# Optimization experiments

Hardware: AMD Instinct MI355X
Metric: run time of the kernel (lower is better)

Reference implementation:

```python
import jax, jax.numpy as jnp
import numpy as np

DIM = 512
N_LABELS = 64


def setup_inputs() -> dict:
    key = jax.random.key(0)
    k1, k2, k3, k4 = jax.random.split(key, 4)
    head = jax.random.normal(k1, (8, 512, DIM), dtype=jnp.float32)
    dep = jax.random.normal(k2, (8, 512, DIM), dtype=jnp.float32)
    label_W = jax.random.normal(k3, (N_LABELS, 2 * DIM), dtype=jnp.float32) * 0.02
    label_b = jax.random.normal(k4, (N_LABELS,), dtype=jnp.float32) * 0.02
    return {"head": head, "dep": dep, "label_W": label_W, "label_b": label_b}


def reference(head, dep, label_W, label_b):
    # Original: concated[b, i*S+j] = concat(head[b,i], dep[b,j]) -> [B, S*S, 2D]
    #           out = (label_W @ concated^T).view(B, L, S, S) + b
    # Fused biaffine decomposition: out[b,l,i,j] = Wh[l].head[b,i] + Wd[l].dep[b,j] + b[l]
    D = head.shape[-1]
    W_head = label_W[:, :D]   # [L, D]
    W_dep = label_W[:, D:]    # [L, D]
    h = jnp.einsum('bid,ld->bli', head, W_head)  # [B, L, S]
    d = jnp.einsum('bjd,ld->blj', dep, W_dep)    # [B, L, S]
    out = h[:, :, :, None] + d[:, :, None, :] + label_b[None, :, None, None]
    return out  # [B, L, S, S]
```

## Files before the change

kernel.cpp:

```cpp
#include <hip/hip_runtime.h>
#include <hip/hip_bf16.h>

#define BATCH 8
#define SEQ   512
#define DIM   512
#define NL    64
#define ITILE 16

typedef float f32x4 __attribute__((ext_vector_type(4)));

__global__ __launch_bounds__(256) void alab_proj(
    const float* __restrict__ head, const float* __restrict__ dep,
    const float* __restrict__ W, const float* __restrict__ bias,
    float* __restrict__ hbuf, float* __restrict__ dbuf)
{
    __shared__ float4 sh[ITILE * (DIM / 4)];
    __shared__ float4 sd[ITILE * (DIM / 4)];
    const int t  = threadIdx.x;
    const int b  = blockIdx.x >> 5;
    const int i0 = (blockIdx.x & 31) * ITILE;

    const float4* h4 = (const float4*)(head + ((size_t)b * SEQ + i0) * DIM);
    const float4* d4 = (const float4*)(dep  + ((size_t)b * SEQ + i0) * DIM);
    #pragma unroll
    for (int u = t; u < ITILE * (DIM / 4); u += 256) {
        const int row = u >> 7, col = u & 127;
        const int sc  = col ^ (row & 7);
        sh[row * 128 + sc] = h4[u];
        sd[row * 128 + sc] = d4[u];
    }
    __syncthreads();

    const int iL = t & 15;
    const int lg = t >> 4;
    const int xm = iL & 7;
    const float4* W4 = (const float4*)W;

    float acch[4] = {0.f, 0.f, 0.f, 0.f};
    float accd[4] = {0.f, 0.f, 0.f, 0.f};
    for (int k4 = 0; k4 < DIM / 4; ++k4) {
        const float4 hv = sh[iL * 128 + (k4 ^ xm)];
        const float4 dv = sd[iL * 128 + (k4 ^ xm)];
        #pragma unroll
        for (int r = 0; r < 4; ++r) {
            const int l = lg * 4 + r;
            const float4 wh = W4[l * 256 + k4];
            const float4 wd = W4[l * 256 + 128 + k4];
            acch[r] += wh.x * hv.x + wh.y * hv.y + wh.z * hv.z + wh.w * hv.w;
            accd[r] += wd.x * dv.x + wd.y * dv.y + wd.z * dv.z + wd.w * dv.w;
        }
    }

    #pragma unroll
    for (int r = 0; r < 4; ++r) {
        const int l = lg * 4 + r;
        const size_t o = ((size_t)b * NL + l) * SEQ + i0 + iL;
        hbuf[o] = acch[r] + bias[l];
        dbuf[o] = accd[r];
    }
}

__global__ __launch_bounds__(256) void alab_bcast3(
    const float* __restrict__ hbuf, const float* __restrict__ dbuf,
    float* __restrict__ out)
{
    __shared__ float sh[SEQ / 4];
    __shared__ f32x4 sd4[SEQ / 4];
    const int t  = threadIdx.x;
    const int q  = blockIdx.x & 3;
    const int bl = blockIdx.x >> 2;

    if (t < 128) sh[t] = hbuf[(size_t)bl * SEQ + q * 128 + t];
    ((float*)sd4)[t]       = dbuf[(size_t)bl * SEQ + t];
    ((float*)sd4)[t + 256] = dbuf[(size_t)bl * SEQ + t + 256];
    __syncthreads();

    const int j4 = t & 127;
    const int rh = t >> 7;
    const f32x4 dreg = sd4[j4];
    f32x4* ob = (f32x4*)out + ((size_t)bl * SEQ + q * 128) * (SEQ / 4);

    #pragma unroll 8
    for (int ii = 0; ii < 128; ii += 2) {
        const int i = ii + rh;
        const f32x4 o = dreg + sh[i];
        ob[(size_t)i * (SEQ / 4) + j4] = o;
    }
}

extern "C" void kernel_launch(void* const* d_in, const int* in_sizes, int n_in,
                              void* d_out, int out_size, void* d_ws, size_t ws_size,
                              hipStream_t stream) {
    const float* head = (const float*)d_in[0];
    const float* dep  = (const float*)d_in[1];
    const float* W    = (const float*)d_in[2];
    const float* bias = (const float*)d_in[3];
    float* out  = (float*)d_out;
    float* hbuf = (float*)d_ws;
    float* dbuf = hbuf + (size_t)BATCH * NL * SEQ;

    alab_proj<<<BATCH * (SEQ / ITILE), 256, 0, stream>>>(head, dep, W, bias, hbuf, dbuf);
    alab_bcast3<<<BATCH * NL * 4, 256, 0, stream>>>(hbuf, dbuf, out);
}
```

Measured before the change: 135.9 us.

## Split projection kernel into separate head/dep blocks with padded LDS and vector accumulators

The projection kernel now launches twice as many blocks, each handling only the head or only the dep half. Each block stages one 16-row tile in padded shared memory instead of an XOR swizzle and accumulates with f32x4 vector FMAs, reducing lanes only at the end. The aim is more parallelism and lower per-block shared memory for the small projection stage. The cost is fewer W loads amortized per block, and the per-block LDS reads change pattern.

```diff
diff --git a/kernel.cpp b/kernel.cpp
--- a/kernel.cpp
+++ b/kernel.cpp
@@ -5,58 +5,60 @@
 #define SEQ   512
 #define DIM   512
 #define NL    64
-#define ITILE 16
 
 typedef float f32x4 __attribute__((ext_vector_type(4)));
 
-__global__ __launch_bounds__(256) void alab_proj(
+__global__ __launch_bounds__(256) void alab_proj2(
     const float* __restrict__ head, const float* __restrict__ dep,
     const float* __restrict__ W, const float* __restrict__ bias,
     float* __restrict__ hbuf, float* __restrict__ dbuf)
 {
-    __shared__ float4 sh[ITILE * (DIM / 4)];
-    __shared__ float4 sd[ITILE * (DIM / 4)];
-    const int t  = threadIdx.x;
-    const int b  = blockIdx.x >> 5;
-    const int i0 = (blockIdx.x & 31) * ITILE;
+    __shared__ float4 srow[16][129];
+    const int bid   = blockIdx.x;
+    const int hd    = bid & 1;
+    const int itile = (bid >> 1) & 31;
+    const int b     = bid >> 6;
+    const int i0    = itile * 16;
 
-    const float4* h4 = (const float4*)(head + ((size_t)b * SEQ + i0) * DIM);
-    const float4* d4 = (const float4*)(dep  + ((size_t)b * SEQ + i0) * DIM);
+    const float* src  = hd ? dep  : head;
+    float*       dst  = hd ? dbuf : hbuf;
+    const int    wofs = hd ? 128  : 0;
+
+    const float4* s4 = (const float4*)(src + ((size_t)b * SEQ + i0) * DIM);
     #pragma unroll
-    for (int u = t; u < ITILE * (DIM / 4); u += 256) {
-        const int row = u >> 7, col = u & 127;
-        const int sc  = col ^ (row & 7);
-        sh[row * 128 + sc] = h4[u];
-        sd[row * 128 + sc] = d4[u];
-    }
+    for (int u = threadIdx.x; u < 16 * 128; u += 256)
+        srow[u >> 7][u & 127] = s4[u];
     __syncthreads();
 
-    const int iL = t & 15;
-    const int lg = t >> 4;
-    const int xm = iL & 7;
-    const float4* W4 = (const float4*)W;
+    const int lane = threadIdx.x & 63;
+    const int w    = threadIdx.x >> 6;
+    const int i    = lane & 15;
+    const int li   = lane >> 4;
+    const int lb   = w * 16 + li * 4;
 
-    float acch[4] = {0.f, 0.f, 0.f, 0.f};
-    float accd[4] = {0.f, 0.f, 0.f, 0.f};
-    for (int k4 = 0; k4 < DIM / 4; ++k4) {
-        const float4 hv = sh[iL * 128 + (k4 ^ xm)];
-        const float4 dv = sd[iL * 128 + (k4 ^ xm)];
-        #pragma unroll
-        for (int r = 0; r < 4; ++r) {
-            const int l = lg * 4 + r;
-            const float4 wh = W4[l * 256 + k4];
-            const float4 wd = W4[l * 256 + 128 + k4];
-            acch[r] += wh.x * hv.x + wh.y * hv.y + wh.z * hv.z + wh.w * hv.w;
-            accd[r] += wd.x * dv.x + wd.y * dv.y + wd.z * dv.z + wd.w * dv.w;
-        }
+    const f32x4* W4 = (const f32x4*)W;
+    f32x4 a0 = {0.f,0.f,0.f,0.f}, a1 = {0.f,0.f,0.f,0.f};
+    f32x4 a2 = {0.f,0.f,0.f,0.f}, a3 = {0.f,0.f,0.f,0.f};
+
+    #pragma unroll 4
+    for (int k4 = 0; k4 < 128; ++k4) {
+        const f32x4 hv = *(const f32x4*)&srow[i][k4];
+        const size_t wb = (size_t)lb * 256 + wofs + k4;
+        a0 += hv * W4[wb];
+        a1 += hv * W4[wb + 256];
+        a2 += hv * W4[wb + 512];
+        a3 += hv * W4[wb + 768];
     }
 
+    float r[4] = { a0.x + a0.y + a0.z + a0.w,
+                   a1.x + a1.y + a1.z + a1.w,
+                   a2.x + a2.y + a2.z + a2.w,
+                   a3.x + a3.y + a3.z + a3.w };
     #pragma unroll
-    for (int r = 0; r < 4; ++r) {
-        const int l = lg * 4 + r;
-        const size_t o = ((size_t)b * NL + l) * SEQ + i0 + iL;
-        hbuf[o] = acch[r] + bias[l];
-        dbuf[o] = accd[r];
+    for (int s = 0; s < 4; ++s) {
+        const int l = lb + s;
+        const float v = r[s] + (hd ? 0.f : bias[l]);
+        dst[((size_t)b * NL + l) * SEQ + i0 + i] = v;
     }
 }
 
@@ -99,6 +101,6 @@
     float* hbuf = (float*)d_ws;
     float* dbuf = hbuf + (size_t)BATCH * NL * SEQ;
 
-    alab_proj<<<BATCH * (SEQ / ITILE), 256, 0, stream>>>(head, dep, W, bias, hbuf, dbuf);
+    alab_proj2<<<BATCH * 32 * 2, 256, 0, stream>>>(head, dep, W, bias, hbuf, dbuf);
     alab_bcast3<<<BATCH * NL * 4, 256, 0, stream>>>(hbuf, dbuf, out);
 }
```

Result: faster. 131.0 us (-3.6%).
